# Optimization experiments

Measured on AMD Instinct MI355X. Metric: run time of the kernel, lower is better.

Reference implementation:

```python
import jax, jax.numpy as jnp
import numpy as np
import math

D_MODEL = 768
N_HEADS = 12
HEAD_DIM = D_MODEL // N_HEADS


def setup_inputs() -> dict:
    key = jax.random.key(0)
    ks = jax.random.split(key, 9)
    B, S = 2, 4096
    scale = 1.0 / math.sqrt(D_MODEL)
    x = jax.random.normal(ks[0], (B, S, D_MODEL), dtype=jnp.float32)
    # Linear weights stored as [in, out] for x @ W; biases [out].
    Wq = jax.random.normal(ks[1], (D_MODEL, D_MODEL), dtype=jnp.float32) * scale
    bq = jax.random.normal(ks[2], (D_MODEL,), dtype=jnp.float32) * 0.01
    Wk = jax.random.normal(ks[3], (D_MODEL, D_MODEL), dtype=jnp.float32) * scale
    bk = jax.random.normal(ks[4], (D_MODEL,), dtype=jnp.float32) * 0.01
    Wv = jax.random.normal(ks[5], (D_MODEL, D_MODEL), dtype=jnp.float32) * scale
    bv = jax.random.normal(ks[6], (D_MODEL,), dtype=jnp.float32) * 0.01
    Wo = jax.random.normal(ks[7], (D_MODEL, D_MODEL), dtype=jnp.float32) * scale
    bo = jax.random.normal(ks[8], (D_MODEL,), dtype=jnp.float32) * 0.01
    return {"x": x, "Wq": Wq, "bq": bq, "Wk": Wk, "bk": bk,
            "Wv": Wv, "bv": bv, "Wo": Wo, "bo": bo}


def reference(x, Wq, bq, Wk, bk, Wv, bv, Wo, bo):
    B, S, _ = x.shape
    def split_heads(t):  # [B,S,D] -> [B,H,S,hd]
        return t.reshape(B, S, N_HEADS, HEAD_DIM).transpose(0, 2, 1, 3)
    Q = split_heads(x @ Wq + bq)
    K = split_heads(x @ Wk + bk)
    V = split_heads(x @ Wv + bv)
    scores = jnp.einsum('bhqd,bhkd->bhqk', Q, K) / math.sqrt(HEAD_DIM)
    attn = jax.nn.softmax(scores, axis=-1)
    ctx = jnp.einsum('bhqk,bhkd->bhqd', attn, V)  # [B,H,S,hd]
    ctx = ctx.transpose(0, 2, 1, 3).reshape(B, S, D_MODEL)
    return ctx @ Wo + bo
```

## Files before the change

kernel.cpp:

```cpp
#include <hip/hip_runtime.h>

typedef __bf16 bf16x8 __attribute__((ext_vector_type(8)));
typedef float f32x4 __attribute__((ext_vector_type(4)));
typedef float f32x16 __attribute__((ext_vector_type(16)));
typedef unsigned short u16x8 __attribute__((ext_vector_type(8)));
typedef unsigned int u32x4 __attribute__((ext_vector_type(4)));

#define DEV static __device__ __forceinline__

DEV unsigned short f2bf(float f) {
  unsigned u = __builtin_bit_cast(unsigned, f);
  u += 0x7fffu + ((u >> 16) & 1u);
  return (unsigned short)(u >> 16);
}
DEV unsigned cvt_pk_bf16(float lo, float hi) {
  unsigned r;
  asm("v_cvt_pk_bf16_f32 %0, %1, %2" : "=v"(r) : "v"(lo), "v"(hi));
  return r;
}
DEV void plswap(unsigned& a, unsigned& b) {
  auto r = __builtin_amdgcn_permlane32_swap(a, b, false, false);
  a = r[0];
  b = r[1];
}
DEV void gload16(const void* g, void* lds) {
  __builtin_amdgcn_global_load_lds(
      (__attribute__((address_space(1))) void*)(g),
      (__attribute__((address_space(3))) void*)(lds), 16, 0, 0);
}

__global__ __launch_bounds__(256) void k_cvt_x(const float* __restrict__ x,
                                               unsigned short* __restrict__ xb) {
  const int i = (blockIdx.x * 256 + threadIdx.x) * 4;
  float4 v = *(const float4*)(x + i);
  ushort4 o;
  o.x = f2bf(v.x); o.y = f2bf(v.y); o.z = f2bf(v.z); o.w = f2bf(v.w);
  *(ushort4*)(xb + i) = o;
}

__global__ __launch_bounds__(256) void k_tw(const float* __restrict__ Wq, const float* __restrict__ Wk,
                                            const float* __restrict__ Wv, const float* __restrict__ Wo,
                                            unsigned short* __restrict__ Wt, unsigned short* __restrict__ Wot) {
  __shared__ float tile[32][33];
  const int z = blockIdx.z;
  const float* W = (z == 0) ? Wq : (z == 1) ? Wk : (z == 2) ? Wv : Wo;
  const int n0 = blockIdx.x * 32, k0 = blockIdx.y * 32;
  const int tx = threadIdx.x, ty = threadIdx.y;
#pragma unroll
  for (int j = 0; j < 4; j++)
    tile[ty + 8 * j][tx] = W[(size_t)(k0 + ty + 8 * j) * 768 + n0 + tx];
  __syncthreads();
  unsigned short* dst = (z == 3) ? Wot : (Wt + (size_t)z * 768 * 768);
#pragma unroll
  for (int j = 0; j < 4; j++)
    dst[(size_t)(n0 + ty + 8 * j) * 768 + k0 + tx] = f2bf(tile[tx][ty + 8 * j]);
}

template <bool F32OUT>
__global__ __launch_bounds__(256, 2) void k_gemm(
    const unsigned short* __restrict__ A, const unsigned short* __restrict__ Bt,
    const float* __restrict__ b0, const float* __restrict__ b1, const float* __restrict__ b2,
    void* __restrict__ out, int M, int K, float scale0) {
  __shared__ char As[8192];
  __shared__ char Bs[8192];
  const int t = threadIdx.x;
  const int l = t & 63, w = t >> 6;
  const int lr = l & 15, lg = l >> 4;
  const int m0 = blockIdx.y * 128, n0 = blockIdx.x * 128;
  const int wr = (w >> 1) * 64, wc = (w & 1) * 64;

  f32x4 acc[4][4];
#pragma unroll
  for (int i = 0; i < 4; i++)
#pragma unroll
    for (int j = 0; j < 4; j++)
#pragma unroll
      for (int r = 0; r < 4; r++) acc[i][j][r] = 0.0f;

  const int rA0 = t >> 2, rA1 = 64 + (t >> 2);
  const int cbl = (t & 3) * 16;
  const int cb0 = cbl ^ ((rA0 & 3) << 4);
  const int cb1 = cbl ^ ((rA1 & 3) << 4);
  const size_t K2 = (size_t)K * 2;
  const char* ga0 = (const char*)A + (size_t)(m0 + rA0) * K2 + cb0;
  const char* ga1 = (const char*)A + (size_t)(m0 + rA1) * K2 + cb1;
  const char* gb0 = (const char*)Bt + (size_t)(n0 + rA0) * K2 + cb0;
  const char* gb1 = (const char*)Bt + (size_t)(n0 + rA1) * K2 + cb1;
  char* AsW = As + w * 1024;
  char* BsW = Bs + w * 1024;

  const int nkt = K >> 5;
  for (int kt = 0; kt < nkt; ++kt) {
    const size_t ko = (size_t)kt * 64;
    gload16(ga0 + ko, AsW);
    gload16(ga1 + ko, AsW + 4096);
    gload16(gb0 + ko, BsW);
    gload16(gb1 + ko, BsW + 4096);
    __syncthreads();
    bf16x8 af[4], bfr[4];
#pragma unroll
    for (int mi = 0; mi < 4; mi++) {
      const int row = wr + mi * 16 + lr;
      af[mi] = *(const bf16x8*)(As + row * 64 + ((lg * 16) ^ ((row & 3) << 4)));
    }
#pragma unroll
    for (int ni = 0; ni < 4; ni++) {
      const int row = wc + ni * 16 + lr;
      bfr[ni] = *(const bf16x8*)(Bs + row * 64 + ((lg * 16) ^ ((row & 3) << 4)));
    }
#pragma unroll
    for (int mi = 0; mi < 4; mi++)
#pragma unroll
      for (int ni = 0; ni < 4; ni++)
        acc[mi][ni] = __builtin_amdgcn_mfma_f32_16x16x32_bf16(af[mi], bfr[ni], acc[mi][ni], 0, 0, 0);
    __syncthreads();
  }

  if constexpr (F32OUT) {
    float* o = (float*)out;
#pragma unroll
    for (int mi = 0; mi < 4; mi++)
#pragma unroll
      for (int ni = 0; ni < 4; ni++) {
        const int col = n0 + wc + ni * 16 + lr;
        const int rowb = m0 + wr + mi * 16 + lg * 4;
        const float bias = b0[col];
#pragma unroll
        for (int r = 0; r < 4; r++)
          o[(size_t)(rowb + r) * 768 + col] = acc[mi][ni][r] + bias;
      }
  } else {
    const int sel = n0 / 768;
    const int cbase = n0 - sel * 768;
    const float* bp = (sel == 0) ? b0 : ((sel == 1) ? b1 : b2);
    const float sc = (sel == 0) ? scale0 : 1.0f;
    unsigned short* o = (unsigned short*)out + (size_t)sel * M * 768;
#pragma unroll
    for (int mi = 0; mi < 4; mi++)
#pragma unroll
      for (int ni = 0; ni < 4; ni++) {
        const int ci = cbase + wc + ni * 16 + lr;
        const int rowb = m0 + wr + mi * 16 + lg * 4;
        const float bias = bp[ci];
#pragma unroll
        for (int r = 0; r < 4; r++)
          o[(size_t)(rowb + r) * 768 + ci] = f2bf((acc[mi][ni][r] + bias) * sc);
      }
  }
}

__global__ __launch_bounds__(256) void k_tv(const unsigned short* __restrict__ V,
                                            unsigned short* __restrict__ Vt) {
  __shared__ unsigned short tile[64][68];
  const int t = threadIdx.x;
  const int s0 = blockIdx.x * 64;
  const int h = blockIdx.y;
  const int b = blockIdx.z;
#pragma unroll
  for (int j = 0; j < 4; j++) {
    const int c = j * 256 + t;
    const int r = c >> 4, cc = c & 15;
    *(ushort4*)(&tile[r][cc * 4]) =
        *(const ushort4*)(V + (size_t)(b * 4096 + s0 + r) * 768 + h * 64 + cc * 4);
  }
  __syncthreads();
#pragma unroll
  for (int j = 0; j < 2; j++) {
    const int c = j * 256 + t;
    const int d = c >> 3, sc = c & 7;
    u16x8 vv;
#pragma unroll
    for (int e = 0; e < 8; e++) vv[e] = tile[sc * 8 + e][d];
    *(u16x8*)(Vt + (size_t)((b * 12 + h) * 64 + d) * 4096 + s0 + sc * 8) = vv;
  }
}

__global__ __launch_bounds__(256, 2) void k_attn(
    const unsigned short* __restrict__ Q, const unsigned short* __restrict__ Kg,
    const unsigned short* __restrict__ Vt, unsigned short* __restrict__ Ctx) {
  __shared__ char Kd[2][8192];
  __shared__ char Vd[2][8192];
  const int t = threadIdx.x;
  const int l = t & 63, w = t >> 6;
  const int lq = l & 31, hi = l >> 5;
  const int bh = blockIdx.x, b = bh / 12, h = bh % 12;
  const int q0 = blockIdx.y * 128 + w * 32;

  bf16x8 qf[4];
  {
    const char* qrow = (const char*)Q + ((size_t)(b * 4096 + q0 + lq) * 768 + h * 64) * 2;
#pragma unroll
    for (int kst = 0; kst < 4; kst++)
      qf[kst] = *(const bf16x8*)(qrow + kst * 32 + hi * 16);
  }

  f32x16 cacc[2];
  f32x16 z16;
#pragma unroll
  for (int r = 0; r < 16; r++) z16[r] = 0.0f;
  cacc[0] = z16; cacc[1] = z16;
  float l_run = 0.0f;

  unsigned koff[2][4];
#pragma unroll
  for (int nt = 0; nt < 2; nt++)
#pragma unroll
    for (int kst = 0; kst < 4; kst++)
      koff[nt][kst] = (unsigned)((nt * 32 + lq) * 128 + ((kst * 32 + hi * 16) ^ ((lq & 7) << 4)));

  const int rS0 = t >> 3, rS1 = 32 + (t >> 3);
  const int cblS = (t & 7) * 16;
  const int cbS0 = cblS ^ ((rS0 & 7) << 4);
  const int cbS1 = cblS ^ ((rS1 & 7) << 4);
  const char* gK0 = (const char*)Kg + ((size_t)(b * 4096 + rS0) * 768 + h * 64) * 2 + cbS0;
  const char* gK1 = (const char*)Kg + ((size_t)(b * 4096 + rS1) * 768 + h * 64) * 2 + cbS1;
  const char* gV0 = (const char*)Vt + ((size_t)(bh * 64 + rS0) * 4096) * 2 + cbS0;
  const char* gV1 = (const char*)Vt + ((size_t)(bh * 64 + rS1) * 4096) * 2 + cbS1;
  char* KdW0 = Kd[0] + w * 1024;
  char* VdW0 = Vd[0] + w * 1024;

  auto STAGE = [&](int buf) {
    gload16(gK0, KdW0 + buf * 8192);
    gload16(gK1, KdW0 + buf * 8192 + 4096);
    gload16(gV0, VdW0 + buf * 8192);
    gload16(gV1, VdW0 + buf * 8192 + 4096);
    gK0 += 98304; gK1 += 98304;
    gV0 += 128;   gV1 += 128;
  };

  auto COMPUTE = [&](const char* Kb, const char* Vb) {
    f32x16 st[2];
    __builtin_amdgcn_s_setprio(1);
#pragma unroll
    for (int nt = 0; nt < 2; nt++) {
      bf16x8 kf0 = *(const bf16x8*)(Kb + koff[nt][0]);
      st[nt] = __builtin_amdgcn_mfma_f32_32x32x16_bf16(kf0, qf[0], z16, 0, 0, 0);
#pragma unroll
      for (int kst = 1; kst < 4; kst++) {
        bf16x8 kf = *(const bf16x8*)(Kb + koff[nt][kst]);
        st[nt] = __builtin_amdgcn_mfma_f32_32x32x16_bf16(kf, qf[kst], st[nt], 0, 0, 0);
      }
    }

    float tsum = 0.0f;
#pragma unroll
    for (int kst = 0; kst < 4; kst++) {
      const f32x16& P = st[kst >> 1];
      const int r0 = (kst & 1) * 8;
      const float e0 = __builtin_amdgcn_exp2f(P[r0 + 0]);
      const float e1 = __builtin_amdgcn_exp2f(P[r0 + 1]);
      const float e2 = __builtin_amdgcn_exp2f(P[r0 + 2]);
      const float e3 = __builtin_amdgcn_exp2f(P[r0 + 3]);
      const float e4 = __builtin_amdgcn_exp2f(P[r0 + 4]);
      const float e5 = __builtin_amdgcn_exp2f(P[r0 + 5]);
      const float e6 = __builtin_amdgcn_exp2f(P[r0 + 6]);
      const float e7 = __builtin_amdgcn_exp2f(P[r0 + 7]);
      tsum += ((e0 + e1) + (e2 + e3)) + ((e4 + e5) + (e6 + e7));
      unsigned A0 = cvt_pk_bf16(e0, e1);
      unsigned A1 = cvt_pk_bf16(e2, e3);
      unsigned B0 = cvt_pk_bf16(e4, e5);
      unsigned B1 = cvt_pk_bf16(e6, e7);
      plswap(A0, B0);
      plswap(A1, B1);
      u32x4 pw; pw[0] = A0; pw[1] = A1; pw[2] = B0; pw[3] = B1;
      const bf16x8 pb = __builtin_bit_cast(bf16x8, pw);
      bf16x8 av0 = *(const bf16x8*)(Vb + koff[0][kst]);
      bf16x8 av1 = *(const bf16x8*)(Vb + koff[1][kst]);
      cacc[0] = __builtin_amdgcn_mfma_f32_32x32x16_bf16(av0, pb, cacc[0], 0, 0, 0);
      cacc[1] = __builtin_amdgcn_mfma_f32_32x32x16_bf16(av1, pb, cacc[1], 0, 0, 0);
    }
    __builtin_amdgcn_s_setprio(0);

    unsigned ua = __builtin_bit_cast(unsigned, tsum), ub = ua;
    plswap(ua, ub);
    l_run += __builtin_bit_cast(float, ua) + __builtin_bit_cast(float, ub);
  };

  STAGE(0);
  __syncthreads();
  for (int kvt = 0; kvt < 64; kvt += 2) {
    STAGE(1);
    COMPUTE(Kd[0], Vd[0]);
    __syncthreads();
    if (kvt + 2 < 64) STAGE(0);
    COMPUTE(Kd[1], Vd[1]);
    __syncthreads();
  }

  char* scratch = Kd[0] + w * 4096;
  const float inv_l = 1.0f / l_run;
#pragma unroll
  for (int ntd = 0; ntd < 2; ntd++)
#pragma unroll
    for (int p4 = 0; p4 < 4; p4++) {
      const unsigned u0 = cvt_pk_bf16(cacc[ntd][p4 * 4 + 0] * inv_l, cacc[ntd][p4 * 4 + 1] * inv_l);
      const unsigned u1 = cvt_pk_bf16(cacc[ntd][p4 * 4 + 2] * inv_l, cacc[ntd][p4 * 4 + 3] * inv_l);
      uint2 uu; uu.x = u0; uu.y = u1;
      *(uint2*)(scratch + lq * 128 + ntd * 64 + p4 * 16 + hi * 8) = uu;
    }
#pragma unroll
  for (int j = 0; j < 4; j++) {
    const int c = j * 64 + l;
    const int qq = c >> 3, c8 = c & 7;
    u16x8 v = *(const u16x8*)(scratch + qq * 128 + c8 * 16);
    *(u16x8*)((char*)Ctx + ((size_t)(b * 4096 + q0 + qq) * 768 + h * 64 + c8 * 8) * 2) = v;
  }
}

extern "C" void kernel_launch(void* const* d_in, const int* in_sizes, int n_in,
                              void* d_out, int out_size, void* d_ws, size_t ws_size,
                              hipStream_t stream) {
  const float* x  = (const float*)d_in[0];
  const float* Wq = (const float*)d_in[1];
  const float* bq = (const float*)d_in[2];
  const float* Wk = (const float*)d_in[3];
  const float* bk = (const float*)d_in[4];
  const float* Wv = (const float*)d_in[5];
  const float* bv = (const float*)d_in[6];
  const float* Wo = (const float*)d_in[7];
  const float* bo = (const float*)d_in[8];

  char* ws = (char*)d_ws;
  unsigned short* Xb  = (unsigned short*)(ws);
  unsigned short* Wt  = (unsigned short*)(ws + 12582912);
  unsigned short* Wot = (unsigned short*)(ws + 16121856);
  unsigned short* QKV = (unsigned short*)(ws + 17301504);
  unsigned short* Vtr = (unsigned short*)(ws + 55050240);
  unsigned short* Ctx = (unsigned short*)(ws + 67633152);
  unsigned short* Qp = QKV;
  unsigned short* Kp = QKV + (size_t)8192 * 768;
  unsigned short* Vp = QKV + (size_t)2 * 8192 * 768;

  const float qscale = 0.18033688011112042f;

  k_cvt_x<<<6144, 256, 0, stream>>>(x, Xb);
  k_tw<<<dim3(24, 24, 4), dim3(32, 8), 0, stream>>>(Wq, Wk, Wv, Wo, Wt, Wot);
  k_gemm<false><<<dim3(18, 64), 256, 0, stream>>>(Xb, Wt, bq, bk, bv, (void*)QKV, 8192, 768, qscale);
  k_tv<<<dim3(64, 12, 2), 256, 0, stream>>>(Vp, Vtr);
  k_attn<<<dim3(24, 32), 256, 0, stream>>>(Qp, Kp, Vtr, Ctx);
  k_gemm<true><<<dim3(6, 64), 256, 0, stream>>>(Ctx, Wot, bo, bo, bo, d_out, 8192, 768, 1.0f);
}
```

Measured before the change: 279.3 us.

## Fuse V transpose into QKV GEMM epilogue, widen K tile, shrink output GEMM tile

Measured after the change: 256.8 us. -8.1%, faster.

```diff
diff --git a/kernel.cpp b/kernel.cpp
--- a/kernel.cpp
+++ b/kernel.cpp
@@ -56,70 +56,82 @@
     dst[(size_t)(n0 + ty + 8 * j) * 768 + k0 + tx] = f2bf(tile[tx][ty + 8 * j]);
 }
 
-template <bool F32OUT>
+template <int BM, bool F32OUT, bool FUSEV>
 __global__ __launch_bounds__(256, 2) void k_gemm(
     const unsigned short* __restrict__ A, const unsigned short* __restrict__ Bt,
     const float* __restrict__ b0, const float* __restrict__ b1, const float* __restrict__ b2,
-    void* __restrict__ out, int M, int K, float scale0) {
-  __shared__ char As[8192];
-  __shared__ char Bs[8192];
+    void* __restrict__ out, unsigned short* __restrict__ Vtr, int M, int K, float scale0) {
+  constexpr int MF = BM / 32;
+  __shared__ char As[BM * 128];
+  __shared__ char Bs[128 * 128];
   const int t = threadIdx.x;
   const int l = t & 63, w = t >> 6;
   const int lr = l & 15, lg = l >> 4;
-  const int m0 = blockIdx.y * 128, n0 = blockIdx.x * 128;
-  const int wr = (w >> 1) * 64, wc = (w & 1) * 64;
-
-  f32x4 acc[4][4];
-#pragma unroll
-  for (int i = 0; i < 4; i++)
+  const int m0 = blockIdx.y * BM, n0 = blockIdx.x * 128;
+  const int wr = (w >> 1) * (BM / 2), wc = (w & 1) * 64;
+
+  f32x4 acc[MF][4];
+#pragma unroll
+  for (int i = 0; i < MF; i++)
 #pragma unroll
     for (int j = 0; j < 4; j++)
 #pragma unroll
       for (int r = 0; r < 4; r++) acc[i][j][r] = 0.0f;
 
-  const int rA0 = t >> 2, rA1 = 64 + (t >> 2);
-  const int cbl = (t & 3) * 16;
-  const int cb0 = cbl ^ ((rA0 & 3) << 4);
-  const int cb1 = cbl ^ ((rA1 & 3) << 4);
   const size_t K2 = (size_t)K * 2;
-  const char* ga0 = (const char*)A + (size_t)(m0 + rA0) * K2 + cb0;
-  const char* ga1 = (const char*)A + (size_t)(m0 + rA1) * K2 + cb1;
-  const char* gb0 = (const char*)Bt + (size_t)(n0 + rA0) * K2 + cb0;
-  const char* gb1 = (const char*)Bt + (size_t)(n0 + rA1) * K2 + cb1;
+  const char* gaj[MF > 2 ? MF : 2];
+  const char* gbj[4];
+#pragma unroll
+  for (int j = 0; j < BM / 32; j++) {
+    const int s = (j * 256 + t) * 16;
+    const int row = s >> 7;
+    const int cb = (s & 127) ^ ((row & 7) << 4);
+    gaj[j] = (const char*)A + (size_t)(m0 + row) * K2 + cb;
+  }
+#pragma unroll
+  for (int j = 0; j < 4; j++) {
+    const int s = (j * 256 + t) * 16;
+    const int row = s >> 7;
+    const int cb = (s & 127) ^ ((row & 7) << 4);
+    gbj[j] = (const char*)Bt + (size_t)(n0 + row) * K2 + cb;
+  }
   char* AsW = As + w * 1024;
   char* BsW = Bs + w * 1024;
 
-  const int nkt = K >> 5;
+  const int nkt = K >> 6;
   for (int kt = 0; kt < nkt; ++kt) {
-    const size_t ko = (size_t)kt * 64;
-    gload16(ga0 + ko, AsW);
-    gload16(ga1 + ko, AsW + 4096);
-    gload16(gb0 + ko, BsW);
-    gload16(gb1 + ko, BsW + 4096);
+    const size_t ko = (size_t)kt * 128;
+#pragma unroll
+    for (int j = 0; j < BM / 32; j++) gload16(gaj[j] + ko, AsW + j * 4096);
+#pragma unroll
+    for (int j = 0; j < 4; j++) gload16(gbj[j] + ko, BsW + j * 4096);
     __syncthreads();
-    bf16x8 af[4], bfr[4];
-#pragma unroll
-    for (int mi = 0; mi < 4; mi++) {
-      const int row = wr + mi * 16 + lr;
-      af[mi] = *(const bf16x8*)(As + row * 64 + ((lg * 16) ^ ((row & 3) << 4)));
-    }
-#pragma unroll
-    for (int ni = 0; ni < 4; ni++) {
-      const int row = wc + ni * 16 + lr;
-      bfr[ni] = *(const bf16x8*)(Bs + row * 64 + ((lg * 16) ^ ((row & 3) << 4)));
-    }
-#pragma unroll
-    for (int mi = 0; mi < 4; mi++)
-#pragma unroll
-      for (int ni = 0; ni < 4; ni++)
-        acc[mi][ni] = __builtin_amdgcn_mfma_f32_16x16x32_bf16(af[mi], bfr[ni], acc[mi][ni], 0, 0, 0);
+#pragma unroll
+    for (int kst = 0; kst < 2; kst++) {
+      bf16x8 af[MF], bfr[4];
+#pragma unroll
+      for (int mi = 0; mi < MF; mi++) {
+        const int row = wr + mi * 16 + lr;
+        af[mi] = *(const bf16x8*)(As + row * 128 + ((kst * 64 + lg * 16) ^ ((row & 7) << 4)));
+      }
+#pragma unroll
+      for (int ni = 0; ni < 4; ni++) {
+        const int row = wc + ni * 16 + lr;
+        bfr[ni] = *(const bf16x8*)(Bs + row * 128 + ((kst * 64 + lg * 16) ^ ((row & 7) << 4)));
+      }
+#pragma unroll
+      for (int mi = 0; mi < MF; mi++)
+#pragma unroll
+        for (int ni = 0; ni < 4; ni++)
+          acc[mi][ni] = __builtin_amdgcn_mfma_f32_16x16x32_bf16(af[mi], bfr[ni], acc[mi][ni], 0, 0, 0);
+    }
     __syncthreads();
   }
 
   if constexpr (F32OUT) {
     float* o = (float*)out;
 #pragma unroll
-    for (int mi = 0; mi < 4; mi++)
+    for (int mi = 0; mi < MF; mi++)
 #pragma unroll
       for (int ni = 0; ni < 4; ni++) {
         const int col = n0 + wc + ni * 16 + lr;
@@ -132,46 +144,39 @@
   } else {
     const int sel = n0 / 768;
     const int cbase = n0 - sel * 768;
-    const float* bp = (sel == 0) ? b0 : ((sel == 1) ? b1 : b2);
-    const float sc = (sel == 0) ? scale0 : 1.0f;
-    unsigned short* o = (unsigned short*)out + (size_t)sel * M * 768;
-#pragma unroll
-    for (int mi = 0; mi < 4; mi++)
-#pragma unroll
-      for (int ni = 0; ni < 4; ni++) {
-        const int ci = cbase + wc + ni * 16 + lr;
-        const int rowb = m0 + wr + mi * 16 + lg * 4;
-        const float bias = bp[ci];
-#pragma unroll
-        for (int r = 0; r < 4; r++)
-          o[(size_t)(rowb + r) * 768 + ci] = f2bf((acc[mi][ni][r] + bias) * sc);
-      }
-  }
-}
-
-__global__ __launch_bounds__(256) void k_tv(const unsigned short* __restrict__ V,
-                                            unsigned short* __restrict__ Vt) {
-  __shared__ unsigned short tile[64][68];
-  const int t = threadIdx.x;
-  const int s0 = blockIdx.x * 64;
-  const int h = blockIdx.y;
-  const int b = blockIdx.z;
-#pragma unroll
-  for (int j = 0; j < 4; j++) {
-    const int c = j * 256 + t;
-    const int r = c >> 4, cc = c & 15;
-    *(ushort4*)(&tile[r][cc * 4]) =
-        *(const ushort4*)(V + (size_t)(b * 4096 + s0 + r) * 768 + h * 64 + cc * 4);
-  }
-  __syncthreads();
-#pragma unroll
-  for (int j = 0; j < 2; j++) {
-    const int c = j * 256 + t;
-    const int d = c >> 3, sc = c & 7;
-    u16x8 vv;
-#pragma unroll
-    for (int e = 0; e < 8; e++) vv[e] = tile[sc * 8 + e][d];
-    *(u16x8*)(Vt + (size_t)((b * 12 + h) * 64 + d) * 4096 + s0 + sc * 8) = vv;
+    if (FUSEV && sel == 2) {
+#pragma unroll
+      for (int mi = 0; mi < MF; mi++)
+#pragma unroll
+        for (int ni = 0; ni < 4; ni++) {
+          const int ci = cbase + wc + ni * 16 + lr;
+          const int h = ci >> 6, d = ci & 63;
+          const float bias = b2[ci];
+          const int rowb = m0 + wr + mi * 16 + lg * 4;
+          const int bb = rowb >> 12, srow = rowb & 4095;
+          ushort4 o4;
+          o4.x = f2bf(acc[mi][ni][0] + bias);
+          o4.y = f2bf(acc[mi][ni][1] + bias);
+          o4.z = f2bf(acc[mi][ni][2] + bias);
+          o4.w = f2bf(acc[mi][ni][3] + bias);
+          *(ushort4*)(Vtr + (((size_t)((bb * 12 + h) * 64 + d)) << 12) + srow) = o4;
+        }
+    } else {
+      const float* bp = (sel == 0) ? b0 : ((sel == 1) ? b1 : b2);
+      const float sc = (sel == 0) ? scale0 : 1.0f;
+      unsigned short* o = (unsigned short*)out + (size_t)sel * M * 768;
+#pragma unroll
+      for (int mi = 0; mi < MF; mi++)
+#pragma unroll
+        for (int ni = 0; ni < 4; ni++) {
+          const int ci = cbase + wc + ni * 16 + lr;
+          const int rowb = m0 + wr + mi * 16 + lg * 4;
+          const float bias = bp[ci];
+#pragma unroll
+          for (int r = 0; r < 4; r++)
+            o[(size_t)(rowb + r) * 768 + ci] = f2bf((acc[mi][ni][r] + bias) * sc);
+        }
+    }
   }
 }
 
@@ -329,14 +334,12 @@
   unsigned short* Ctx = (unsigned short*)(ws + 67633152);
   unsigned short* Qp = QKV;
   unsigned short* Kp = QKV + (size_t)8192 * 768;
-  unsigned short* Vp = QKV + (size_t)2 * 8192 * 768;
 
   const float qscale = 0.18033688011112042f;
 
   k_cvt_x<<<6144, 256, 0, stream>>>(x, Xb);
   k_tw<<<dim3(24, 24, 4), dim3(32, 8), 0, stream>>>(Wq, Wk, Wv, Wo, Wt, Wot);
-  k_gemm<false><<<dim3(18, 64), 256, 0, stream>>>(Xb, Wt, bq, bk, bv, (void*)QKV, 8192, 768, qscale);
-  k_tv<<<dim3(64, 12, 2), 256, 0, stream>>>(Vp, Vtr);
+  k_gemm<128, false, true><<<dim3(18, 64), 256, 0, stream>>>(Xb, Wt, bq, bk, bv, (void*)QKV, Vtr, 8192, 768, qscale);
   k_attn<<<dim3(24, 32), 256, 0, stream>>>(Qp, Kp, Vtr, Ctx);
-  k_gemm<true><<<dim3(6, 64), 256, 0, stream>>>(Ctx, Wot, bo, bo, bo, d_out, 8192, 768, 1.0f);
-}
+  k_gemm<64, true, false><<<dim3(6, 128), 256, 0, stream>>>(Ctx, Wot, bo, bo, bo, d_out, nullptr, 8192, 768, 1.0f);
+}
```
